# Kernel tuning notes

Measured on AMD Instinct MI355X. Metric: run time of the kernel, lower is better.

## Reference

```python
import jax, jax.numpy as jnp
import numpy as np

N_NODES = 50000
N_EDGES = 800000
F_IN = 256
F_OUT = 256


def setup_inputs() -> dict:
    key = jax.random.key(0)
    k1, k2, k3, k4, k5 = jax.random.split(key, 5)
    x = jax.random.normal(k1, (N_NODES, F_IN), dtype=jnp.float32)
    edge_index = jax.random.randint(k2, (2, N_EDGES), 0, N_NODES, dtype=jnp.int64)
    C_values = jax.random.uniform(k3, (N_EDGES,), dtype=jnp.float32)
    # nn.Linear(input_dim, output_dim) parameters
    W = jax.random.normal(k4, (F_OUT, F_IN), dtype=jnp.float32) / np.sqrt(F_IN)
    b = jax.random.normal(k5, (F_OUT,), dtype=jnp.float32) * 0.01
    return {"x": x, "edge_index": edge_index, "C_values": C_values, "W": W, "b": b}


def reference(x, edge_index, C_values, W, b):
    # gcn_norm(add_self_loops=False): deg = row-sum of edge weights,
    # w_norm[e] = deg[row]^-1/2 * w[e] * deg[col]^-1/2
    row, col = edge_index[0], edge_index[1]
    n = x.shape[0]
    deg = jax.ops.segment_sum(C_values, row, num_segments=n)  # [N]
    deg_inv_sqrt = jnp.where(deg > 0, jax.lax.rsqrt(jnp.where(deg > 0, deg, 1.0)), 0.0)
    w_norm = deg_inv_sqrt[row] * C_values * deg_inv_sqrt[col]  # [E]
    # SpMM: prop_x[i] = sum_{e: row[e]=i} w_norm[e] * x[col[e]]
    prop_x = jax.ops.segment_sum(w_norm[:, None] * x[col], row, num_segments=n)  # [N, F_in]
    # dense linear transform
    return prop_x @ W.T + b  # [N, F_out]
```

## Files before the change

kernel.cpp:

```cpp
#include <hip/hip_runtime.h>
#include <hip/hip_bf16.h>

#define NN 50000
#define NE 800000
#define FD 256
#define NN_PAD 50048
#define SCAN_B 196
#define NPB 16

typedef __attribute__((ext_vector_type(8))) short bf16x8;
typedef __attribute__((ext_vector_type(4))) float f32x4;
typedef unsigned long long ull;

__device__ __forceinline__ short f2bf(float f) {
    union { float f; unsigned u; } v; v.f = f;
    unsigned r = v.u + 0x7fffu + ((v.u >> 16) & 1u);
    return (short)(r >> 16);
}
__device__ __forceinline__ float bf2f(unsigned short u) {
    union { unsigned u; float f; } v; v.u = ((unsigned)u) << 16;
    return v.f;
}

__global__ void count_deg_kernel(const int* __restrict__ row, const float* __restrict__ cv,
                                 ull* __restrict__ dc) {
    int e = blockIdx.x * blockDim.x + threadIdx.x;
    if (e < NE) {
        int r = row[e];
        unsigned cf = (unsigned)(cv[e] * 16777216.0f + 0.5f);
        atomicAdd(&dc[r], (1ULL << 40) | (ull)cf);
    }
}

__device__ __forceinline__ int block_excl_scan256(int v, int tid) {
    __shared__ int ws[4];
    int lane = tid & 63, wv = tid >> 6;
    int incl = v;
#pragma unroll
    for (int off = 1; off < 64; off <<= 1) {
        int t = __shfl_up(incl, off);
        if (lane >= off) incl += t;
    }
    if (lane == 63) ws[wv] = incl;
    __syncthreads();
    int acc = 0;
#pragma unroll
    for (int k = 0; k < 4; ++k) if (k < wv) acc += ws[k];
    return acc + incl - v;
}

__global__ void sum_dinv_kernel(const ull* __restrict__ dc, float* __restrict__ dinv,
                                int* __restrict__ bsum) {
    int i = blockIdx.x * 256 + threadIdx.x;
    ull v = (i < NN) ? dc[i] : 0ULL;
    int cnt = (int)(v >> 40);
    ull df = v & ((1ULL << 40) - 1);
    int lane = threadIdx.x & 63, wv = threadIdx.x >> 6;
    int s = cnt;
#pragma unroll
    for (int off = 1; off < 64; off <<= 1) s += __shfl_xor(s, off);
    __shared__ int ws[4];
    if (lane == 0) ws[wv] = s;
    __syncthreads();
    if (threadIdx.x == 0) bsum[blockIdx.x] = ws[0] + ws[1] + ws[2] + ws[3];
    if (i < NN) {
        float d = (float)df * (1.0f / 16777216.0f);
        dinv[i] = (df > 0) ? rsqrtf(d) : 0.f;
    }
}

__global__ void scan_bsum_kernel(int* __restrict__ bsum) {
    int tid = threadIdx.x;
    int v = (tid < SCAN_B) ? bsum[tid] : 0;
    int excl = block_excl_scan256(v, tid);
    if (tid < SCAN_B) bsum[tid] = excl;
}

__global__ void write_rs_kernel(const ull* __restrict__ dc, const int* __restrict__ bsum,
                                int* __restrict__ rs, int* __restrict__ cursor) {
    int i = blockIdx.x * 256 + threadIdx.x;
    int v = (i < NN) ? (int)(dc[i] >> 40) : 0;
    int excl = block_excl_scan256(v, threadIdx.x) + bsum[blockIdx.x];
    if (i < NN) { rs[i] = excl; cursor[i] = excl; }
    if (i == NN - 1) rs[NN] = excl + v;
}

__global__ void quant_kernel(const float* __restrict__ x, const float* __restrict__ W,
                             const float* __restrict__ dinv, unsigned* __restrict__ q8,
                             float* __restrict__ scale, short* __restrict__ Wb) {
    int wid = blockIdx.x * 4 + (threadIdx.x >> 6);
    int lane = threadIdx.x & 63;
    if (wid < NN) {
        int r = wid;
        float dr = dinv[r];
        float4 v = *(const float4*)(x + (size_t)r * FD + lane * 4);
        v.x *= dr; v.y *= dr; v.z *= dr; v.w *= dr;
        float m = fmaxf(fmaxf(fabsf(v.x), fabsf(v.y)), fmaxf(fabsf(v.z), fabsf(v.w)));
#pragma unroll
        for (int off = 1; off < 64; off <<= 1) m = fmaxf(m, __shfl_xor(m, off, 64));
        float s   = (m > 0.f) ? m * (1.0f / 127.0f) : 1.0f;
        float inv = (m > 0.f) ? 127.0f / m : 0.f;
        if (lane == 0) scale[r] = s;
        int q0 = (int)rintf(v.x * inv) + 128;
        int q1 = (int)rintf(v.y * inv) + 128;
        int q2 = (int)rintf(v.z * inv) + 128;
        int q3 = (int)rintf(v.w * inv) + 128;
        q8[r * 64 + lane] = (unsigned)q0 | ((unsigned)q1 << 8) |
                            ((unsigned)q2 << 16) | ((unsigned)q3 << 24);
    } else {
        int j = (wid - NN) * 64 + lane;
        if (j < FD * FD) Wb[j] = f2bf(W[j]);
    }
}

__global__ void bucket_kernel(const int* __restrict__ row, const int* __restrict__ col,
                              const float* __restrict__ cv, const float* __restrict__ scale,
                              int* __restrict__ cursor, unsigned* __restrict__ e_cw) {
    int e = blockIdx.x * blockDim.x + threadIdx.x;
    if (e >= NE) return;
    int r = row[e], c = col[e];
    float w = cv[e] * scale[c];
    int idx = atomicAdd(&cursor[r], 1);
    unsigned wb = (unsigned)(unsigned short)f2bf(w);
    e_cw[idx] = (wb << 16) | (unsigned)c;
}

__global__ __launch_bounds__(256) void fused_kernel(
        const unsigned* __restrict__ q8, const unsigned* __restrict__ e_cw,
        const int* __restrict__ rs, const float* __restrict__ dinv,
        const short* __restrict__ Wb, const float* __restrict__ bias,
        float* __restrict__ out) {
    __shared__ short Ab[NPB][264];
    int tid = threadIdx.x, lane = tid & 63, wv = tid >> 6;
    int q = lane >> 4, i = lane & 15;
    int nbase = blockIdx.x * NPB;
    int n = nbase + wv * 4 + q;

    int e = rs[n], en = rs[n + 1];
    const unsigned* xq = q8 + i * 4;

    float acc[16];
#pragma unroll
    for (int k = 0; k < 16; ++k) acc[k] = 0.f;
    float wsum = 0.f;

#define EDGE(V, CW) do {                                                     \
        float w_ = bf2f((unsigned short)((CW) >> 16));                       \
        wsum += w_;                                                          \
        acc[0]  = fmaf(w_, (float)(unsigned char)((V).x      ), acc[0]);     \
        acc[1]  = fmaf(w_, (float)(unsigned char)((V).x >>  8), acc[1]);     \
        acc[2]  = fmaf(w_, (float)(unsigned char)((V).x >> 16), acc[2]);     \
        acc[3]  = fmaf(w_, (float)((V).x >> 24), acc[3]);                    \
        acc[4]  = fmaf(w_, (float)(unsigned char)((V).y      ), acc[4]);     \
        acc[5]  = fmaf(w_, (float)(unsigned char)((V).y >>  8), acc[5]);     \
        acc[6]  = fmaf(w_, (float)(unsigned char)((V).y >> 16), acc[6]);     \
        acc[7]  = fmaf(w_, (float)((V).y >> 24), acc[7]);                    \
        acc[8]  = fmaf(w_, (float)(unsigned char)((V).z      ), acc[8]);     \
        acc[9]  = fmaf(w_, (float)(unsigned char)((V).z >>  8), acc[9]);     \
        acc[10] = fmaf(w_, (float)(unsigned char)((V).z >> 16), acc[10]);    \
        acc[11] = fmaf(w_, (float)((V).z >> 24), acc[11]);                   \
        acc[12] = fmaf(w_, (float)(unsigned char)((V).w      ), acc[12]);    \
        acc[13] = fmaf(w_, (float)(unsigned char)((V).w >>  8), acc[13]);    \
        acc[14] = fmaf(w_, (float)(unsigned char)((V).w >> 16), acc[14]);    \
        acc[15] = fmaf(w_, (float)((V).w >> 24), acc[15]);                   \
    } while (0)

    while (e < en && (e & 3)) {
        unsigned cw = e_cw[e];
        uint4 v = *(const uint4*)(xq + (size_t)(cw & 0xFFFFu) * 64);
        EDGE(v, cw);
        ++e;
    }
    for (; e + 4 <= en; e += 4) {
        uint4 cw4 = *(const uint4*)(e_cw + e);
        uint4 v0 = *(const uint4*)(xq + (size_t)(cw4.x & 0xFFFFu) * 64);
        uint4 v1 = *(const uint4*)(xq + (size_t)(cw4.y & 0xFFFFu) * 64);
        uint4 v2 = *(const uint4*)(xq + (size_t)(cw4.z & 0xFFFFu) * 64);
        uint4 v3 = *(const uint4*)(xq + (size_t)(cw4.w & 0xFFFFu) * 64);
        EDGE(v0, cw4.x);
        EDGE(v1, cw4.y);
        EDGE(v2, cw4.z);
        EDGE(v3, cw4.w);
    }
    for (; e < en; ++e) {
        unsigned cw = e_cw[e];
        uint4 v = *(const uint4*)(xq + (size_t)(cw & 0xFFFFu) * 64);
        EDGE(v, cw);
    }
#undef EDGE

    {
        float dr = dinv[n];
        float base = 128.f * wsum;
        bf16x8 lo, hi;
#pragma unroll
        for (int k = 0; k < 8; ++k) {
            lo[k] = f2bf((acc[k] - base) * dr);
            hi[k] = f2bf((acc[k + 8] - base) * dr);
        }
        *(bf16x8*)&Ab[wv * 4 + q][i * 16] = lo;
        *(bf16x8*)&Ab[wv * 4 + q][i * 16 + 8] = hi;
    }
    __syncthreads();

    int m = lane & 15, g = lane >> 4;
    f32x4 acc0 = {0,0,0,0}, acc1 = {0,0,0,0}, acc2 = {0,0,0,0}, acc3 = {0,0,0,0};
    const short* w0 = Wb + (size_t)(wv * 64 + 0  + m) * FD;
    const short* w1 = Wb + (size_t)(wv * 64 + 16 + m) * FD;
    const short* w2 = Wb + (size_t)(wv * 64 + 32 + m) * FD;
    const short* w3 = Wb + (size_t)(wv * 64 + 48 + m) * FD;
#pragma unroll
    for (int ks = 0; ks < 8; ++ks) {
        int ko = ks * 32 + g * 8;
        bf16x8 af = *(const bf16x8*)&Ab[m][ko];
        bf16x8 b0 = *(const bf16x8*)(w0 + ko);
        bf16x8 b1 = *(const bf16x8*)(w1 + ko);
        bf16x8 b2 = *(const bf16x8*)(w2 + ko);
        bf16x8 b3 = *(const bf16x8*)(w3 + ko);
        acc0 = __builtin_amdgcn_mfma_f32_16x16x32_bf16(af, b0, acc0, 0, 0, 0);
        acc1 = __builtin_amdgcn_mfma_f32_16x16x32_bf16(af, b1, acc1, 0, 0, 0);
        acc2 = __builtin_amdgcn_mfma_f32_16x16x32_bf16(af, b2, acc2, 0, 0, 0);
        acc3 = __builtin_amdgcn_mfma_f32_16x16x32_bf16(af, b3, acc3, 0, 0, 0);
    }
#pragma unroll
    for (int nt = 0; nt < 4; ++nt) {
        f32x4 a = nt == 0 ? acc0 : nt == 1 ? acc1 : nt == 2 ? acc2 : acc3;
        int c = wv * 64 + nt * 16 + m;
        float bv = bias[c];
#pragma unroll
        for (int r = 0; r < 4; ++r) {
            out[(size_t)(nbase + g * 4 + r) * FD + c] = a[r] + bv;
        }
    }
}

extern "C" void kernel_launch(void* const* d_in, const int* in_sizes, int n_in,
                              void* d_out, int out_size, void* d_ws, size_t ws_size,
                              hipStream_t stream) {
    const float* x  = (const float*)d_in[0];
    const int*   ei = (const int*)d_in[1];
    const float* cv = (const float*)d_in[2];
    const float* W  = (const float*)d_in[3];
    const float* b  = (const float*)d_in[4];
    float* out = (float*)d_out;

    const int* row = ei;
    const int* col = ei + NE;

    ull*      dc     = (ull*)d_ws;
    unsigned* e_cw   = (unsigned*)(dc + NN_PAD);
    unsigned* q8     = e_cw + NE;
    short*    Wb     = (short*)(q8 + (size_t)NN * 64);
    float*    dinv   = (float*)(Wb + (size_t)FD * FD);
    float*    scale  = dinv + NN_PAD;
    int*      rs     = (int*)(scale + NN_PAD);
    int*      cursor = rs + NN_PAD;
    int*      bsum   = cursor + NN_PAD;

    hipMemsetAsync(dc, 0, NN_PAD * sizeof(ull), stream);

    count_deg_kernel<<<(NE + 255) / 256, 256, 0, stream>>>(row, cv, dc);
    sum_dinv_kernel<<<SCAN_B, 256, 0, stream>>>(dc, dinv, bsum);
    scan_bsum_kernel<<<1, 256, 0, stream>>>(bsum);
    write_rs_kernel<<<SCAN_B, 256, 0, stream>>>(dc, bsum, rs, cursor);
    quant_kernel<<<NN / 4 + 256, 256, 0, stream>>>(x, W, dinv, q8, scale, Wb);
    bucket_kernel<<<(NE + 255) / 256, 256, 0, stream>>>(row, col, cv, scale, cursor, e_cw);

    fused_kernel<<<NN / NPB, 256, 0, stream>>>(q8, e_cw, rs, dinv, Wb, b, out);
}
```

Before: 187.0 us.

## Fold block-sum scan into write_rs, unroll edge gather by 8, add nontemporal hints

Drops the single-block scan kernel: each write_rs block now redundantly scans the 196 block sums in shared memory, which saves one launch. The fused SpMM kernel gets an 8-edge unrolled gather loop so more independent x-row loads are in flight. It also uses nontemporal loads for the edge stream and nontemporal stores for the output, and adds an occupancy hint of 6 waves in launch_bounds. The risks are higher register pressure from the larger unroll being capped by the occupancy hint, and redundant scan work in every block.

```diff
diff --git a/kernel.cpp b/kernel.cpp
--- a/kernel.cpp
+++ b/kernel.cpp
@@ -10,6 +10,7 @@
 
 typedef __attribute__((ext_vector_type(8))) short bf16x8;
 typedef __attribute__((ext_vector_type(4))) float f32x4;
+typedef __attribute__((ext_vector_type(4))) unsigned uintx4;
 typedef unsigned long long ull;
 
 __device__ __forceinline__ short f2bf(float f) {
@@ -69,18 +70,17 @@
     }
 }
 
-__global__ void scan_bsum_kernel(int* __restrict__ bsum) {
-    int tid = threadIdx.x;
-    int v = (tid < SCAN_B) ? bsum[tid] : 0;
-    int excl = block_excl_scan256(v, tid);
-    if (tid < SCAN_B) bsum[tid] = excl;
-}
-
 __global__ void write_rs_kernel(const ull* __restrict__ dc, const int* __restrict__ bsum,
                                 int* __restrict__ rs, int* __restrict__ cursor) {
-    int i = blockIdx.x * 256 + threadIdx.x;
+    __shared__ int sb[SCAN_B];
+    int tid = threadIdx.x;
+    int bv = (tid < SCAN_B) ? bsum[tid] : 0;
+    int excl_b = block_excl_scan256(bv, tid);
+    if (tid < SCAN_B) sb[tid] = excl_b;
+    __syncthreads();
+    int i = blockIdx.x * 256 + tid;
     int v = (i < NN) ? (int)(dc[i] >> 40) : 0;
-    int excl = block_excl_scan256(v, threadIdx.x) + bsum[blockIdx.x];
+    int excl = block_excl_scan256(v, tid) + sb[blockIdx.x];
     if (i < NN) { rs[i] = excl; cursor[i] = excl; }
     if (i == NN - 1) rs[NN] = excl + v;
 }
@@ -125,7 +125,7 @@
     e_cw[idx] = (wb << 16) | (unsigned)c;
 }
 
-__global__ __launch_bounds__(256) void fused_kernel(
+__global__ __launch_bounds__(256, 6) void fused_kernel(
         const unsigned* __restrict__ q8, const unsigned* __restrict__ e_cw,
         const int* __restrict__ rs, const float* __restrict__ dinv,
         const short* __restrict__ Wb, const float* __restrict__ bias,
@@ -171,8 +171,28 @@
         EDGE(v, cw);
         ++e;
     }
+    for (; e + 8 <= en; e += 8) {
+        uintx4 cwA = __builtin_nontemporal_load((const uintx4*)(e_cw + e));
+        uintx4 cwB = __builtin_nontemporal_load((const uintx4*)(e_cw + e + 4));
+        uint4 v0 = *(const uint4*)(xq + (size_t)(cwA.x & 0xFFFFu) * 64);
+        uint4 v1 = *(const uint4*)(xq + (size_t)(cwA.y & 0xFFFFu) * 64);
+        uint4 v2 = *(const uint4*)(xq + (size_t)(cwA.z & 0xFFFFu) * 64);
+        uint4 v3 = *(const uint4*)(xq + (size_t)(cwA.w & 0xFFFFu) * 64);
+        uint4 v4 = *(const uint4*)(xq + (size_t)(cwB.x & 0xFFFFu) * 64);
+        uint4 v5 = *(const uint4*)(xq + (size_t)(cwB.y & 0xFFFFu) * 64);
+        uint4 v6 = *(const uint4*)(xq + (size_t)(cwB.z & 0xFFFFu) * 64);
+        uint4 v7 = *(const uint4*)(xq + (size_t)(cwB.w & 0xFFFFu) * 64);
+        EDGE(v0, cwA.x);
+        EDGE(v1, cwA.y);
+        EDGE(v2, cwA.z);
+        EDGE(v3, cwA.w);
+        EDGE(v4, cwB.x);
+        EDGE(v5, cwB.y);
+        EDGE(v6, cwB.z);
+        EDGE(v7, cwB.w);
+    }
     for (; e + 4 <= en; e += 4) {
-        uint4 cw4 = *(const uint4*)(e_cw + e);
+        uintx4 cw4 = __builtin_nontemporal_load((const uintx4*)(e_cw + e));
         uint4 v0 = *(const uint4*)(xq + (size_t)(cw4.x & 0xFFFFu) * 64);
         uint4 v1 = *(const uint4*)(xq + (size_t)(cw4.y & 0xFFFFu) * 64);
         uint4 v2 = *(const uint4*)(xq + (size_t)(cw4.z & 0xFFFFu) * 64);
@@ -229,7 +249,8 @@
         float bv = bias[c];
 #pragma unroll
         for (int r = 0; r < 4; ++r) {
-            out[(size_t)(nbase + g * 4 + r) * FD + c] = a[r] + bv;
+            __builtin_nontemporal_store(a[r] + bv,
+                &out[(size_t)(nbase + g * 4 + r) * FD + c]);
         }
     }
 }
@@ -261,7 +282,6 @@
 
     count_deg_kernel<<<(NE + 255) / 256, 256, 0, stream>>>(row, cv, dc);
     sum_dinv_kernel<<<SCAN_B, 256, 0, stream>>>(dc, dinv, bsum);
-    scan_bsum_kernel<<<1, 256, 0, stream>>>(bsum);
     write_rs_kernel<<<SCAN_B, 256, 0, stream>>>(dc, bsum, rs, cursor);
     quant_kernel<<<NN / 4 + 256, 256, 0, stream>>>(x, W, dinv, q8, scale, Wb);
     bucket_kernel<<<(NE + 255) / 256, 256, 0, stream>>>(row, col, cv, scale, cursor, e_cw);
```

Measured after the change: 200.1 us. 7.0% more time.
